# Kernel optimization log

Hardware: AMD Instinct MI355X
Metric: run time of the kernel (lower is better)

## Reference

```python
import jax, jax.numpy as jnp
import numpy as np

B, T, V, D = 128, 512, 8000, 256
H = D // 2   # per-direction LSTM hidden
L = 4        # label_dim


def setup_inputs() -> dict:
    key = jax.random.key(0)
    ks = jax.random.split(key, 16)
    s = 0.1
    pad_seq = jax.random.randint(ks[0], (B, T), 0, V)
    lens = jax.random.randint(ks[1], (B,), 1, T + 1)
    lens = lens.at[0].set(T)  # padded length == max(lens), as pad_packed_sequence would give
    emb = (jax.random.normal(ks[2], (V, D)) * s).at[0].set(0.0)  # padding_idx=0
    return {
        "pad_seq": pad_seq, "lens": lens, "emb": emb,
        "W_ih_f": jax.random.normal(ks[3], (4 * H, D)) * s,
        "W_hh_f": jax.random.normal(ks[4], (4 * H, H)) * s,
        "b_ih_f": jax.random.normal(ks[5], (4 * H,)) * s,
        "b_hh_f": jax.random.normal(ks[6], (4 * H,)) * s,
        "W_ih_b": jax.random.normal(ks[7], (4 * H, D)) * s,
        "W_hh_b": jax.random.normal(ks[8], (4 * H, H)) * s,
        "b_ih_b": jax.random.normal(ks[9], (4 * H,)) * s,
        "b_hh_b": jax.random.normal(ks[10], (4 * H,)) * s,
        "W_lab": jax.random.normal(ks[11], (L, D)) * s,
        "b_lab": jax.random.normal(ks[12], (L,)) * s,
        "transitions": jax.random.normal(ks[13], (L, L)),
        "from_BOS": jax.random.normal(ks[14], (L,)),
        "to_EOS": jax.random.normal(ks[15], (L,)),
    }


def _lstm(xs_t, mask_t, Wih, Whh, bih, bhh, reverse):
    """Masked unidirectional LSTM over time-major xs_t [T,B,D]; emulates
    pack_padded_sequence semantics (state frozen and output zeroed at pads)."""
    nb, nh = xs_t.shape[1], Whh.shape[1]

    def step(carry, inp):
        h, c = carry
        x_t, m_t = inp  # [B,D], [B,1] bool
        g = x_t @ Wih.T + bih + h @ Whh.T + bhh
        i, f, gg, o = jnp.split(g, 4, axis=-1)
        c2 = jax.nn.sigmoid(f) * c + jax.nn.sigmoid(i) * jnp.tanh(gg)
        h2 = jax.nn.sigmoid(o) * jnp.tanh(c2)
        h = jnp.where(m_t, h2, h)
        c = jnp.where(m_t, c2, c)
        return (h, c), jnp.where(m_t, h2, 0.0)

    init = (jnp.zeros((nb, nh), xs_t.dtype), jnp.zeros((nb, nh), xs_t.dtype))
    _, ys = jax.lax.scan(step, init, (xs_t, mask_t), reverse=reverse)
    return ys  # [T,B,H]


def reference(pad_seq, lens, emb, W_ih_f, W_hh_f, b_ih_f, b_hh_f,
              W_ih_b, W_hh_b, b_ih_b, b_hh_b, W_lab, b_lab,
              transitions, from_BOS, to_EOS):
    b, t = pad_seq.shape
    x = emb[pad_seq]                       # [B,T,D]
    xs_t = jnp.transpose(x, (1, 0, 2))     # [T,B,D]
    mask_t = (jnp.arange(t)[:, None] < lens[None, :])[:, :, None]  # [T,B,1]

    hf = _lstm(xs_t, mask_t, W_ih_f, W_hh_f, b_ih_f, b_hh_f, reverse=False)
    hb = _lstm(xs_t, mask_t, W_ih_b, W_hh_b, b_ih_b, b_hh_b, reverse=True)
    h = jnp.concatenate([hf, hb], axis=-1)           # [T,B,D]
    scores = h @ W_lab.T + b_lab                     # [T,B,L] emissions

    # --- Viterbi forward pass ---
    best0 = from_BOS[None, :] + scores[0]            # [B,L]

    def vstep(best, inp):
        ti, e = inp                                  # step index, emissions [B,L]
        smat = best[:, :, None] + e[:, None, :] + transitions[None]  # [B,prev,cur]
        valid = (lens > ti)[:, None]
        nb = jnp.where(valid, smat.max(axis=1), best)
        return nb, jnp.argmax(smat, axis=1)          # backtrace [B,L]

    bestT, bt = jax.lax.scan(vstep, best0, (jnp.arange(1, t), scores[1:]))
    final_vec = bestT + to_EOS[None, :]              # [B,L]
    last_lab = jnp.argmax(final_vec, axis=1)         # [B]

    # --- backtrace: label[t] = bt[t][label[t+1]] for t < len-1 ---
    bt_pad = jnp.concatenate([bt, jnp.zeros((1,) + bt.shape[1:], bt.dtype)], axis=0)  # [T,B,L]

    def bstep(cur, inp):
        ti, bt_t = inp
        cand = jnp.take_along_axis(bt_t, cur[:, None], axis=1)[:, 0]
        cur = jnp.where(ti == lens - 1, last_lab,
                        jnp.where(ti < lens - 1, cand, cur))
        return cur, cur

    _, labs = jax.lax.scan(bstep, jnp.zeros((b,), last_lab.dtype),
                           (jnp.arange(t), bt_pad), reverse=True)
    labels = labs.T  # [B,T]
    len_bool = jnp.arange(t)[None, :] < lens[:, None]
    return labels * len_bool
```

## Files before the change

kernel.cpp:

```cpp
#include <hip/hip_runtime.h>
#include <math.h>

#define VOCAB 8000
#define BATCH 128
#define TMAX  512
#define DIM   256
#define HID   128
#define G4    512
#define NCOL  1024

__device__ __forceinline__ float dpp_xor1(float x) {
  int r = __builtin_amdgcn_update_dpp(0, __builtin_bit_cast(int, x),
                                      0xB1, 0xF, 0xF, true);
  return __builtin_bit_cast(float, r);
}
__device__ __forceinline__ float dpp_xor2(float x) {
  int r = __builtin_amdgcn_update_dpp(0, __builtin_bit_cast(int, x),
                                      0x4E, 0xF, 0xF, true);
  return __builtin_bit_cast(float, r);
}
__device__ __forceinline__ unsigned dpp_xor1u(unsigned x) {
  return (unsigned)__builtin_amdgcn_update_dpp(0, (int)x, 0xB1, 0xF, 0xF, true);
}
__device__ __forceinline__ unsigned dpp_xor2u(unsigned x) {
  return (unsigned)__builtin_amdgcn_update_dpp(0, (int)x, 0x4E, 0xF, 0xF, true);
}
__device__ __forceinline__ float dpp_bc0(float x) {
  int r = __builtin_amdgcn_update_dpp(0, __builtin_bit_cast(int, x),
                                      0x00, 0xF, 0xF, true);
  return __builtin_bit_cast(float, r);
}
__device__ __forceinline__ float dpp_bc1(float x) {
  int r = __builtin_amdgcn_update_dpp(0, __builtin_bit_cast(int, x),
                                      0x55, 0xF, 0xF, true);
  return __builtin_bit_cast(float, r);
}
__device__ __forceinline__ float dpp_bc2(float x) {
  int r = __builtin_amdgcn_update_dpp(0, __builtin_bit_cast(int, x),
                                      0xAA, 0xF, 0xF, true);
  return __builtin_bit_cast(float, r);
}
__device__ __forceinline__ float dpp_bc3(float x) {
  int r = __builtin_amdgcn_update_dpp(0, __builtin_bit_cast(int, x),
                                      0xFF, 0xF, 0xF, true);
  return __builtin_bit_cast(float, r);
}

__device__ __forceinline__ void bar_lds() {
  asm volatile("s_waitcnt lgkmcnt(0)" ::: "memory");
  __builtin_amdgcn_s_barrier();
}

__global__ __launch_bounds__(256) void embw_gemm(
    const float* __restrict__ emb,
    const float* __restrict__ Wf, const float* __restrict__ Wb,
    const float* __restrict__ bihf, const float* __restrict__ bhhf,
    const float* __restrict__ bihb, const float* __restrict__ bhhb,
    float* __restrict__ embW) {
  __shared__ float As[32][132];
  __shared__ float Bs[32][132];
  const int tid = threadIdx.x;
  const int m0 = blockIdx.x * 128;
  const int n0 = blockIdx.y * 128;
  const int tx = tid & 15, ty = tid >> 4;
  const int lrow = tid >> 1;
  const int lseg = (tid & 1) * 16;
  const float* Wsrc = (n0 < 512) ? Wf : Wb;
  const int nbase = (n0 < 512) ? n0 : (n0 - 512);

  float acc[8][8];
  #pragma unroll
  for (int i = 0; i < 8; ++i)
    #pragma unroll
    for (int jj = 0; jj < 8; ++jj) acc[i][jj] = 0.f;

  for (int k0 = 0; k0 < 256; k0 += 32) {
    const int gm = m0 + lrow;
    #pragma unroll
    for (int q = 0; q < 4; ++q) {
      float4 v = make_float4(0.f, 0.f, 0.f, 0.f);
      if (gm < VOCAB) v = *(const float4*)(emb + (size_t)gm * 256 + k0 + lseg + 4 * q);
      As[lseg + 4*q + 0][lrow] = v.x;
      As[lseg + 4*q + 1][lrow] = v.y;
      As[lseg + 4*q + 2][lrow] = v.z;
      As[lseg + 4*q + 3][lrow] = v.w;
    }
    #pragma unroll
    for (int q = 0; q < 4; ++q) {
      float4 v = *(const float4*)(Wsrc + (size_t)(nbase + lrow) * 256 + k0 + lseg + 4 * q);
      Bs[lseg + 4*q + 0][lrow] = v.x;
      Bs[lseg + 4*q + 1][lrow] = v.y;
      Bs[lseg + 4*q + 2][lrow] = v.z;
      Bs[lseg + 4*q + 3][lrow] = v.w;
    }
    __syncthreads();
    #pragma unroll
    for (int k = 0; k < 32; ++k) {
      float4 av0 = *(const float4*)&As[k][ty * 8];
      float4 av1 = *(const float4*)&As[k][ty * 8 + 4];
      float4 bv0 = *(const float4*)&Bs[k][tx * 4];
      float4 bv1 = *(const float4*)&Bs[k][64 + tx * 4];
      float a[8]  = {av0.x, av0.y, av0.z, av0.w, av1.x, av1.y, av1.z, av1.w};
      float bb[8] = {bv0.x, bv0.y, bv0.z, bv0.w, bv1.x, bv1.y, bv1.z, bv1.w};
      #pragma unroll
      for (int i = 0; i < 8; ++i)
        #pragma unroll
        for (int jj = 0; jj < 8; ++jj)
          acc[i][jj] += a[i] * bb[jj];
    }
    __syncthreads();
  }

  float bias[8];
  #pragma unroll
  for (int jj = 0; jj < 8; ++jj) {
    int n = n0 + ((jj < 4) ? (tx * 4 + jj) : (64 + tx * 4 + (jj - 4)));
    bias[jj] = (n < 512) ? (bihf[n] + bhhf[n]) : (bihb[n - 512] + bhhb[n - 512]);
  }
  #pragma unroll
  for (int i = 0; i < 8; ++i) {
    int gm = m0 + ty * 8 + i;
    if (gm >= VOCAB) continue;
    float4 v0 = make_float4(acc[i][0] + bias[0], acc[i][1] + bias[1],
                            acc[i][2] + bias[2], acc[i][3] + bias[3]);
    float4 v1 = make_float4(acc[i][4] + bias[4], acc[i][5] + bias[5],
                            acc[i][6] + bias[6], acc[i][7] + bias[7]);
    *(float4*)(embW + (size_t)gm * NCOL + n0 + tx * 4) = v0;
    *(float4*)(embW + (size_t)gm * NCOL + n0 + 64 + tx * 4) = v1;
  }
}

#define REP8(M) M(0) M(1) M(2) M(3) M(4) M(5) M(6) M(7)
#define REP8G(M,G) M(G,0) M(G,1) M(G,2) M(G,3) M(G,4) M(G,5) M(G,6) M(G,7)

__global__ __launch_bounds__(512)
__attribute__((amdgpu_waves_per_eu(2, 2)))
void lstm_rec(
    const int* __restrict__ pad_seq, const int* __restrict__ lens,
    const float* __restrict__ Whh_f, const float* __restrict__ Whh_b,
    const float* __restrict__ embW, const float* __restrict__ W_lab,
    float* __restrict__ e_part) {
  const int dir = blockIdx.x & 1;
  const int b   = blockIdx.x >> 1;
  const int tid = threadIdx.x;
  const int j   = tid >> 2;
  const int q   = tid & 3;
  const int parity = q & 1;
  const int half   = (q >> 1) & 1;

  __shared__ float ring[8][4][36];
  __shared__ float wls[4][132];
  __shared__ int   tok[TMAX];

  tok[tid] = pad_seq[b * TMAX + tid];
  wls[tid >> 7][tid & 127] = W_lab[(tid >> 7) * DIM + dir * HID + (tid & 127)];
  if (tid < 144) ((float*)ring)[tid] = 0.f;

  const int len = lens[b];
  const float* __restrict__ Whh = dir ? Whh_b : Whh_f;

  const float4* wr0 = (const float4*)(Whh + (size_t)(0 * HID + j) * HID + 32 * q);
  const float4* wr1 = (const float4*)(Whh + (size_t)(1 * HID + j) * HID + 32 * q);
  const float4* wr2 = (const float4*)(Whh + (size_t)(2 * HID + j) * HID + 32 * q);
  const float4* wr3 = (const float4*)(Whh + (size_t)(3 * HID + j) * HID + 32 * q);
#define DECLW(G,I)                                                      \
  float w##G##_##I##_0, w##G##_##I##_1, w##G##_##I##_2, w##G##_##I##_3; \
  { float4 t = wr##G[I];                                                \
    w##G##_##I##_0 = t.x; w##G##_##I##_1 = t.y;                         \
    w##G##_##I##_2 = t.z; w##G##_##I##_3 = t.w; }                       \
  asm volatile("" : "+v"(w##G##_##I##_0));                              \
  asm volatile("" : "+v"(w##G##_##I##_1));                              \
  asm volatile("" : "+v"(w##G##_##I##_2));                              \
  asm volatile("" : "+v"(w##G##_##I##_3));
  REP8G(DECLW,0) REP8G(DECLW,1) REP8G(DECLW,2) REP8G(DECLW,3)
#undef DECLW

#define KEEPW(G,I)                                                      \
  asm volatile("" : "+v"(w##G##_##I##_0), "+v"(w##G##_##I##_1),         \
                    "+v"(w##G##_##I##_2), "+v"(w##G##_##I##_3));

  float c = 0.f;
  const float ascale = (q == 2) ? 2.f : 1.f;
  const float* __restrict__ ecol = embW + dir * G4 + (q * HID + j);
  float* __restrict__ ep = e_part + (size_t)(dir * BATCH + b) * TMAX * 4;

  bar_lds();

  float xb0, xb1, xb2, xb3, xb4, xb5, xb6, xb7;
#define PRE(r) { const int ss = nbase + r; xb##r = 0.f;                 \
    if (ss < len) {                                                     \
      const int tt = dir ? (len - 1 - ss) : ss;                         \
      xb##r = ecol[(size_t)tok[tt] * NCOL]; } }
  { const int nbase = 0; REP8(PRE) }

#define MACC(G,I)                                         \
    a##G##0 = fmaf(hv##I.x, w##G##_##I##_0, a##G##0);     \
    a##G##1 = fmaf(hv##I.y, w##G##_##I##_1, a##G##1);     \
    a##G##2 = fmaf(hv##I.z, w##G##_##I##_2, a##G##2);     \
    a##G##3 = fmaf(hv##I.w, w##G##_##I##_3, a##G##3);

#define STEP(r, XW)                                                     \
  {                                                                     \
    const float4* h4 = (const float4*)&ring[r][q][0];                   \
    float4 hv0 = h4[0], hv1 = h4[1], hv2 = h4[2], hv3 = h4[3];          \
    float4 hv4 = h4[4], hv5 = h4[5], hv6 = h4[6], hv7 = h4[7];          \
    float a00=0.f,a01=0.f,a02=0.f,a03=0.f;                              \
    float a10=0.f,a11=0.f,a12=0.f,a13=0.f;                              \
    float a20=0.f,a21=0.f,a22=0.f,a23=0.f;                              \
    float a30=0.f,a31=0.f,a32=0.f,a33=0.f;                              \
    REP8G(MACC,0) REP8G(MACC,1) REP8G(MACC,2) REP8G(MACC,3)             \
    const float p0 = (a00+a01)+(a02+a03);                               \
    const float p1 = (a10+a11)+(a12+a13);                               \
    const float p2 = (a20+a21)+(a22+a23);                               \
    const float p3 = (a30+a31)+(a32+a33);                               \
     \
    const float klo = parity ? p1 : p0, slo = parity ? p0 : p1;         \
    const float khi = parity ? p3 : p2, shi = parity ? p2 : p3;         \
    const float alo = klo + dpp_xor1(slo);                              \
    const float ahi = khi + dpp_xor1(shi);                              \
    const float kb = half ? ahi : alo, sb = half ? alo : ahi;           \
    const float tot = kb + dpp_xor2(sb);                                \
    const float aa = tot + (XW);                                        \
    const float sg = 1.f / (1.f + __expf(-ascale * aa));                \
    const float act = (q == 2) ? (2.f * sg - 1.f) : sg;                 \
                          \
    const float e1 = dpp_xor1(act);                                     \
    const float e2 = dpp_xor2(act);                                     \
    const float e3 = dpp_xor2(e1);                                      \
    const float ev  = parity ? e1 : act, od  = parity ? act : e1;       \
    const float ev2 = parity ? e3 : e2,  od2 = parity ? e2 : e3;        \
    const float ig = half ? ev2 : ev, fg = half ? od2 : od;             \
    const float gt = half ? ev : ev2, og = half ? od : od2;             \
    c = fg * c + ig * gt;                                               \
    const float s2 = 1.f / (1.f + __expf(-2.f * c));                    \
    const float hh = og * (2.f * s2 - 1.f);                             \
    if (q == 0) ring[(r + 1) & 7][j >> 5][j & 31] = hh;                 \
    bar_lds();                                                          \
  }

  for (int s0 = 0; s0 < len; s0 += 8) {
    REP8G(KEEPW,0) REP8G(KEEPW,1) REP8G(KEEPW,2) REP8G(KEEPW,3)
    const int cnt = (len - s0 < 8) ? (len - s0) : 8;
    STEP(0, xb0)
    if (cnt > 1) STEP(1, xb1)
    if (cnt > 2) STEP(2, xb2)
    if (cnt > 3) STEP(3, xb3)
    if (cnt > 4) STEP(4, xb4)
    if (cnt > 5) STEP(5, xb5)
    if (cnt > 6) STEP(6, xb6)
    if (cnt > 7) STEP(7, xb7)
    { const int nbase = s0 + 8; REP8(PRE) }
    {
      const int r = tid >> 6, l = (tid >> 4) & 3, sub = tid & 15;
      if (r < cnt) {
        const float4* hp = (const float4*)&ring[(r + 1) & 7][sub >> 2][8 * (sub & 3)];
        const float4 h0 = hp[0], h1 = hp[1];
        const float4* wp = (const float4*)&wls[l][8 * sub];
        const float4 u0 = wp[0], u1 = wp[1];
        float d = h0.x*u0.x + h0.y*u0.y + h0.z*u0.z + h0.w*u0.w
                + h1.x*u1.x + h1.y*u1.y + h1.z*u1.z + h1.w*u1.w;
        d += dpp_xor1(d); d += dpp_xor2(d);
        d += __shfl_xor(d, 4); d += __shfl_xor(d, 8);
        if (sub == 0) {
          const int ss = s0 + r;
          const int tt = dir ? (len - 1 - ss) : ss;
          ep[tt * 4 + l] = d;
        }
      }
    }
    bar_lds();
  }
#undef STEP
#undef MACC
#undef PRE
#undef KEEPW
}

__global__ __launch_bounds__(512) void viterbi_k(
    const int* __restrict__ lens, const float* __restrict__ e_part,
    const float* __restrict__ b_lab, const float* __restrict__ trans,
    const float* __restrict__ from_BOS, const float* __restrict__ to_EOS,
    int* __restrict__ out) {
  const int b = blockIdx.x;
  const int tid = threadIdx.x;
  __shared__ float sc[TMAX][4];
  __shared__ unsigned btm[TMAX];
  __shared__ int labs[TMAX];
  const int len = lens[b];

  if (tid < len) {
    const float4 f  = *(const float4*)(e_part + ((size_t)b * TMAX + tid) * 4);
    const float4 g2 = *(const float4*)(e_part + ((size_t)(BATCH + b) * TMAX + tid) * 4);
    const float4 bl = *(const float4*)b_lab;
    sc[tid][0] = f.x + g2.x + bl.x;
    sc[tid][1] = f.y + g2.y + bl.y;
    sc[tid][2] = f.z + g2.z + bl.z;
    sc[tid][3] = f.w + g2.w + bl.w;
  }
  __syncthreads();

  if (tid < 4) {
    const int l = tid;
    float trc0 = trans[0 * 4 + l], trc1 = trans[1 * 4 + l];
    float trc2 = trans[2 * 4 + l], trc3 = trans[3 * 4 + l];
    float best = from_BOS[l] + sc[0][l];
    float e_next = sc[1][l];
    for (int ti = 1; ti < len; ++ti) {
      const float e = e_next;
      e_next = sc[(ti + 1 < TMAX) ? ti + 1 : ti][l];
      const float b0 = dpp_bc0(best);
      const float b1 = dpp_bc1(best);
      const float b2 = dpp_bc2(best);
      const float b3 = dpp_bc3(best);
      float m = (b0 + e) + trc0; int arg = 0;
      float v;
      v = (b1 + e) + trc1; if (v > m) { m = v; arg = 1; }
      v = (b2 + e) + trc2; if (v > m) { m = v; arg = 2; }
      v = (b3 + e) + trc3; if (v > m) { m = v; arg = 3; }
      best = m;
      unsigned av = ((unsigned)arg) << (8 * l);
      av |= dpp_xor1u(av);
      av |= dpp_xor2u(av);
      if (l == 0) btm[ti] = av;
    }
    const float f0 = dpp_bc0(best) + to_EOS[0];
    const float f1 = dpp_bc1(best) + to_EOS[1];
    const float f2 = dpp_bc2(best) + to_EOS[2];
    const float f3 = dpp_bc3(best) + to_EOS[3];
    if (l == 0) {
      float m = f0; int last = 0;
      if (f1 > m) { m = f1; last = 1; }
      if (f2 > m) { m = f2; last = 2; }
      if (f3 > m) { m = f3; last = 3; }
      labs[len - 1] = last;
      int cur = last;
      #pragma unroll 4
      for (int ti = len - 2; ti >= 0; --ti) {
        cur = (int)((btm[ti + 1] >> (8 * cur)) & 255u);
        labs[ti] = cur;
      }
    }
  }
  __syncthreads();
  out[b * TMAX + tid] = (tid < len) ? labs[tid] : 0;
}

extern "C" void kernel_launch(void* const* d_in, const int* in_sizes, int n_in,
                              void* d_out, int out_size, void* d_ws, size_t ws_size,
                              hipStream_t stream) {
  const int*   pad_seq  = (const int*)d_in[0];
  const int*   lens     = (const int*)d_in[1];
  const float* emb      = (const float*)d_in[2];
  const float* W_ih_f   = (const float*)d_in[3];
  const float* W_hh_f   = (const float*)d_in[4];
  const float* b_ih_f   = (const float*)d_in[5];
  const float* b_hh_f   = (const float*)d_in[6];
  const float* W_ih_b   = (const float*)d_in[7];
  const float* W_hh_b   = (const float*)d_in[8];
  const float* b_ih_b   = (const float*)d_in[9];
  const float* b_hh_b   = (const float*)d_in[10];
  const float* W_lab    = (const float*)d_in[11];
  const float* b_lab    = (const float*)d_in[12];
  const float* trans    = (const float*)d_in[13];
  const float* from_BOS = (const float*)d_in[14];
  const float* to_EOS   = (const float*)d_in[15];
  int* out = (int*)d_out;

  float* embW   = (float*)d_ws;
  float* e_part = embW + (size_t)VOCAB * NCOL;

  embw_gemm<<<dim3(63, 8), 256, 0, stream>>>(emb, W_ih_f, W_ih_b,
                                             b_ih_f, b_hh_f, b_ih_b, b_hh_b, embW);
  lstm_rec<<<dim3(2 * BATCH), 512, 0, stream>>>(pad_seq, lens, W_hh_f, W_hh_b,
                                                embW, W_lab, e_part);
  viterbi_k<<<dim3(BATCH), 512, 0, stream>>>(lens, e_part, b_lab, trans,
                                             from_BOS, to_EOS, out);
}
```

Before: 577.3 us.

## Repartition LSTM recurrent matvec to two hidden units per 8-lane group

Each 8-lane group now computes two hidden units, with every lane holding a 16-wide K slice for all four gates of both units. Previously each 4-lane group handled one unit over a 32-wide slice. The h vector in LDS is re-laid out with padding per 16-wide slice, so each lane reads 4 float4s instead of 8. The cross-lane reduction gains a third stage, done with a ds_swizzle xor-4, and the output-projection shuffles also switch to ds_swizzle. The aim is to halve per-step LDS reads of h, at the cost of a longer reduction chain and serial FMA dependence chains per accumulator.

```diff
diff --git a/kernel.cpp b/kernel.cpp
--- a/kernel.cpp
+++ b/kernel.cpp
@@ -43,6 +43,14 @@
 __device__ __forceinline__ float dpp_bc3(float x) {
   int r = __builtin_amdgcn_update_dpp(0, __builtin_bit_cast(int, x),
                                       0xFF, 0xF, 0xF, true);
+  return __builtin_bit_cast(float, r);
+}
+__device__ __forceinline__ float swz_xor4(float x) {
+  int r = __builtin_amdgcn_ds_swizzle(__builtin_bit_cast(int, x), 0x101F);
+  return __builtin_bit_cast(float, r);
+}
+__device__ __forceinline__ float swz_xor8(float x) {
+  int r = __builtin_amdgcn_ds_swizzle(__builtin_bit_cast(int, x), 0x201F);
   return __builtin_bit_cast(float, r);
 }
 
@@ -131,7 +139,9 @@
 }
 
 #define REP8(M) M(0) M(1) M(2) M(3) M(4) M(5) M(6) M(7)
-#define REP8G(M,G) M(G,0) M(G,1) M(G,2) M(G,3) M(G,4) M(G,5) M(G,6) M(G,7)
+#define REPI(M,G,U) M(G,U,0) M(G,U,1) M(G,U,2) M(G,U,3)
+#define REPROW(M) REPI(M,0,0) REPI(M,1,0) REPI(M,2,0) REPI(M,3,0) \
+                  REPI(M,0,1) REPI(M,1,1) REPI(M,2,1) REPI(M,3,1)
 
 __global__ __launch_bounds__(512)
 __attribute__((amdgpu_waves_per_eu(2, 2)))
@@ -143,46 +153,53 @@
   const int dir = blockIdx.x & 1;
   const int b   = blockIdx.x >> 1;
   const int tid = threadIdx.x;
-  const int j   = tid >> 2;
-  const int q   = tid & 3;
-  const int parity = q & 1;
-  const int half   = (q >> 1) & 1;
-
-  __shared__ float ring[8][4][36];
+  const int oct = tid & 7;
+  const int grp2 = 2 * (tid >> 3);
+  const int o0 = oct & 1, o1b = (oct >> 1) & 1, o2b = (oct >> 2) & 1;
+  const int q = oct & 3;
+  const int parity = o0;
+  const int half   = o1b;
+
+  __shared__ float ring[8][160];
   __shared__ float wls[4][132];
   __shared__ int   tok[TMAX];
 
   tok[tid] = pad_seq[b * TMAX + tid];
   wls[tid >> 7][tid & 127] = W_lab[(tid >> 7) * DIM + dir * HID + (tid & 127)];
-  if (tid < 144) ((float*)ring)[tid] = 0.f;
+  if (tid < 160) ((float*)ring)[tid] = 0.f;
 
   const int len = lens[b];
   const float* __restrict__ Whh = dir ? Whh_b : Whh_f;
 
-  const float4* wr0 = (const float4*)(Whh + (size_t)(0 * HID + j) * HID + 32 * q);
-  const float4* wr1 = (const float4*)(Whh + (size_t)(1 * HID + j) * HID + 32 * q);
-  const float4* wr2 = (const float4*)(Whh + (size_t)(2 * HID + j) * HID + 32 * q);
-  const float4* wr3 = (const float4*)(Whh + (size_t)(3 * HID + j) * HID + 32 * q);
-#define DECLW(G,I)                                                      \
-  float w##G##_##I##_0, w##G##_##I##_1, w##G##_##I##_2, w##G##_##I##_3; \
-  { float4 t = wr##G[I];                                                \
-    w##G##_##I##_0 = t.x; w##G##_##I##_1 = t.y;                         \
-    w##G##_##I##_2 = t.z; w##G##_##I##_3 = t.w; }                       \
-  asm volatile("" : "+v"(w##G##_##I##_0));                              \
-  asm volatile("" : "+v"(w##G##_##I##_1));                              \
-  asm volatile("" : "+v"(w##G##_##I##_2));                              \
-  asm volatile("" : "+v"(w##G##_##I##_3));
-  REP8G(DECLW,0) REP8G(DECLW,1) REP8G(DECLW,2) REP8G(DECLW,3)
+#define DECLROW(G,U)                                                    \
+  const float4* wr##G##U = (const float4*)(Whh +                        \
+      (size_t)((G) * HID + grp2 + (U)) * HID + 16 * oct);
+  DECLROW(0,0) DECLROW(1,0) DECLROW(2,0) DECLROW(3,0)
+  DECLROW(0,1) DECLROW(1,1) DECLROW(2,1) DECLROW(3,1)
+#undef DECLROW
+#define DECLW(G,U,I)                                                    \
+  float w##G##U##_##I##_0, w##G##U##_##I##_1,                           \
+        w##G##U##_##I##_2, w##G##U##_##I##_3;                           \
+  { float4 t = wr##G##U[I];                                             \
+    w##G##U##_##I##_0 = t.x; w##G##U##_##I##_1 = t.y;                   \
+    w##G##U##_##I##_2 = t.z; w##G##U##_##I##_3 = t.w; }                 \
+  asm volatile("" : "+v"(w##G##U##_##I##_0));                           \
+  asm volatile("" : "+v"(w##G##U##_##I##_1));                           \
+  asm volatile("" : "+v"(w##G##U##_##I##_2));                           \
+  asm volatile("" : "+v"(w##G##U##_##I##_3));
+  REPROW(DECLW)
 #undef DECLW
 
-#define KEEPW(G,I)                                                      \
-  asm volatile("" : "+v"(w##G##_##I##_0), "+v"(w##G##_##I##_1),         \
-                    "+v"(w##G##_##I##_2), "+v"(w##G##_##I##_3));
+#define KEEPW(G,U,I)                                                    \
+  asm volatile("" : "+v"(w##G##U##_##I##_0), "+v"(w##G##U##_##I##_1),   \
+                    "+v"(w##G##U##_##I##_2), "+v"(w##G##U##_##I##_3));
 
   float c = 0.f;
   const float ascale = (q == 2) ? 2.f : 1.f;
-  const float* __restrict__ ecol = embW + dir * G4 + (q * HID + j);
+  const float* __restrict__ ecol = embW + dir * G4 + q * HID + grp2 + o2b;
   float* __restrict__ ep = e_part + (size_t)(dir * BATCH + b) * TMAX * 4;
+  const int nunit = grp2 + o2b;
+  const int hoff  = 20 * (nunit >> 4) + (nunit & 15);
 
   bar_lds();
 
@@ -193,33 +210,35 @@
       xb##r = ecol[(size_t)tok[tt] * NCOL]; } }
   { const int nbase = 0; REP8(PRE) }
 
-#define MACC(G,I)                                         \
-    a##G##0 = fmaf(hv##I.x, w##G##_##I##_0, a##G##0);     \
-    a##G##1 = fmaf(hv##I.y, w##G##_##I##_1, a##G##1);     \
-    a##G##2 = fmaf(hv##I.z, w##G##_##I##_2, a##G##2);     \
-    a##G##3 = fmaf(hv##I.w, w##G##_##I##_3, a##G##3);
+#define MACC(G,U,I)                                                     \
+    a##G##U = fmaf(hv##I.x, w##G##U##_##I##_0, a##G##U);                \
+    a##G##U = fmaf(hv##I.y, w##G##U##_##I##_1, a##G##U);                \
+    a##G##U = fmaf(hv##I.z, w##G##U##_##I##_2, a##G##U);                \
+    a##G##U = fmaf(hv##I.w, w##G##U##_##I##_3, a##G##U);
 
 #define STEP(r, XW)                                                     \
   {                                                                     \
-    const float4* h4 = (const float4*)&ring[r][q][0];                   \
+    const float4* h4 = (const float4*)&ring[r][20 * oct];               \
     float4 hv0 = h4[0], hv1 = h4[1], hv2 = h4[2], hv3 = h4[3];          \
-    float4 hv4 = h4[4], hv5 = h4[5], hv6 = h4[6], hv7 = h4[7];          \
-    float a00=0.f,a01=0.f,a02=0.f,a03=0.f;                              \
-    float a10=0.f,a11=0.f,a12=0.f,a13=0.f;                              \
-    float a20=0.f,a21=0.f,a22=0.f,a23=0.f;                              \
-    float a30=0.f,a31=0.f,a32=0.f,a33=0.f;                              \
-    REP8G(MACC,0) REP8G(MACC,1) REP8G(MACC,2) REP8G(MACC,3)             \
-    const float p0 = (a00+a01)+(a02+a03);                               \
-    const float p1 = (a10+a11)+(a12+a13);                               \
-    const float p2 = (a20+a21)+(a22+a23);                               \
-    const float p3 = (a30+a31)+(a32+a33);                               \
-     \
-    const float klo = parity ? p1 : p0, slo = parity ? p0 : p1;         \
-    const float khi = parity ? p3 : p2, shi = parity ? p2 : p3;         \
-    const float alo = klo + dpp_xor1(slo);                              \
-    const float ahi = khi + dpp_xor1(shi);                              \
-    const float kb = half ? ahi : alo, sb = half ? alo : ahi;           \
-    const float tot = kb + dpp_xor2(sb);                                \
+    float a00=0.f,a10=0.f,a20=0.f,a30=0.f;                              \
+    float a01=0.f,a11=0.f,a21=0.f,a31=0.f;                              \
+    REPROW(MACC)                                                        \
+                  \
+    float t0, t1;                                                       \
+    t0 = o0 ? a10 : a00; t1 = o0 ? a00 : a10;                           \
+    const float b0 = t0 + dpp_xor1(t1);                                 \
+    t0 = o0 ? a30 : a20; t1 = o0 ? a20 : a30;                           \
+    const float b1 = t0 + dpp_xor1(t1);                                 \
+    t0 = o0 ? a11 : a01; t1 = o0 ? a01 : a11;                           \
+    const float b2 = t0 + dpp_xor1(t1);                                 \
+    t0 = o0 ? a31 : a21; t1 = o0 ? a21 : a31;                           \
+    const float b3 = t0 + dpp_xor1(t1);                                 \
+    t0 = o1b ? b1 : b0; t1 = o1b ? b0 : b1;                             \
+    const float c0s = t0 + dpp_xor2(t1);                                \
+    t0 = o1b ? b3 : b2; t1 = o1b ? b2 : b3;                             \
+    const float c1s = t0 + dpp_xor2(t1);                                \
+    t0 = o2b ? c1s : c0s; t1 = o2b ? c0s : c1s;                         \
+    const float tot = t0 + swz_xor4(t1);                                \
     const float aa = tot + (XW);                                        \
     const float sg = 1.f / (1.f + __expf(-ascale * aa));                \
     const float act = (q == 2) ? (2.f * sg - 1.f) : sg;                 \
@@ -234,12 +253,12 @@
     c = fg * c + ig * gt;                                               \
     const float s2 = 1.f / (1.f + __expf(-2.f * c));                    \
     const float hh = og * (2.f * s2 - 1.f);                             \
-    if (q == 0) ring[(r + 1) & 7][j >> 5][j & 31] = hh;                 \
+    if (q == 0) ring[(r + 1) & 7][hoff] = hh;                           \
     bar_lds();                                                          \
   }
 
   for (int s0 = 0; s0 < len; s0 += 8) {
-    REP8G(KEEPW,0) REP8G(KEEPW,1) REP8G(KEEPW,2) REP8G(KEEPW,3)
+    REPROW(KEEPW)
     const int cnt = (len - s0 < 8) ? (len - s0) : 8;
     STEP(0, xb0)
     if (cnt > 1) STEP(1, xb1)
@@ -253,14 +272,15 @@
     {
       const int r = tid >> 6, l = (tid >> 4) & 3, sub = tid & 15;
       if (r < cnt) {
-        const float4* hp = (const float4*)&ring[(r + 1) & 7][sub >> 2][8 * (sub & 3)];
+        const float4* hp = (const float4*)
+            &ring[(r + 1) & 7][20 * (sub >> 1) + 8 * (sub & 1)];
         const float4 h0 = hp[0], h1 = hp[1];
         const float4* wp = (const float4*)&wls[l][8 * sub];
         const float4 u0 = wp[0], u1 = wp[1];
         float d = h0.x*u0.x + h0.y*u0.y + h0.z*u0.z + h0.w*u0.w
                 + h1.x*u1.x + h1.y*u1.y + h1.z*u1.z + h1.w*u1.w;
         d += dpp_xor1(d); d += dpp_xor2(d);
-        d += __shfl_xor(d, 4); d += __shfl_xor(d, 8);
+        d += swz_xor4(d); d += swz_xor8(d);
         if (sub == 0) {
           const int ss = s0 + r;
           const int tt = dir ? (len - 1 - ss) : ss;
```

Measured after the change: 578.1 us. No clear change (+0.1%).

## Split each LSTM gate's hidden-state dot product across two threads

Applied to the files above, without the earlier changes.

The recurrent kernel now runs 1024 threads per block instead of 512. Eight threads serve each hidden unit: each handles one gate and half of the 128-long recurrent dot product, so it holds 64 recurrent weights in registers instead of 128. This halves the serial FMA chain per thread on the per-step critical path. A single DPP add combines the two halves, and the gate exchange now uses xor-2 and xor-4 lane swizzles, adding a new helper. In exchange, every per-step barrier must synchronise twice as many waves, and more threads repeat the nonlinearities.

```diff
diff --git a/kernel.cpp b/kernel.cpp
--- a/kernel.cpp
+++ b/kernel.cpp
@@ -17,6 +17,12 @@
 __device__ __forceinline__ float dpp_xor2(float x) {
   int r = __builtin_amdgcn_update_dpp(0, __builtin_bit_cast(int, x),
                                       0x4E, 0xF, 0xF, true);
+  return __builtin_bit_cast(float, r);
+}
+__device__ __forceinline__ float dpp_xor4(float x) {
+  int t = __builtin_amdgcn_update_dpp(0, __builtin_bit_cast(int, x),
+                                      0x1B, 0xF, 0xF, true);
+  int r = __builtin_amdgcn_update_dpp(0, t, 0x141, 0xF, 0xF, true);
   return __builtin_bit_cast(float, r);
 }
 __device__ __forceinline__ unsigned dpp_xor1u(unsigned x) {
@@ -131,10 +137,10 @@
 }
 
 #define REP8(M) M(0) M(1) M(2) M(3) M(4) M(5) M(6) M(7)
-#define REP8G(M,G) M(G,0) M(G,1) M(G,2) M(G,3) M(G,4) M(G,5) M(G,6) M(G,7)
-
-__global__ __launch_bounds__(512)
-__attribute__((amdgpu_waves_per_eu(2, 2)))
+#define REP16(M) M(0) M(1) M(2) M(3) M(4) M(5) M(6) M(7) \
+                 M(8) M(9) M(10) M(11) M(12) M(13) M(14) M(15)
+
+__global__ __launch_bounds__(1024, 4)
 void lstm_rec(
     const int* __restrict__ pad_seq, const int* __restrict__ lens,
     const float* __restrict__ Whh_f, const float* __restrict__ Whh_b,
@@ -143,45 +149,44 @@
   const int dir = blockIdx.x & 1;
   const int b   = blockIdx.x >> 1;
   const int tid = threadIdx.x;
-  const int j   = tid >> 2;
-  const int q   = tid & 3;
-  const int parity = q & 1;
-  const int half   = (q >> 1) & 1;
+  const int j   = tid >> 3;
+  const int s   = tid & 7;
+  const int g   = s >> 1;
+  const int kh  = s & 1;
+  const int parity = g & 1;
+  const int half   = g >> 1;
 
   __shared__ float ring[8][4][36];
   __shared__ float wls[4][132];
   __shared__ int   tok[TMAX];
 
-  tok[tid] = pad_seq[b * TMAX + tid];
-  wls[tid >> 7][tid & 127] = W_lab[(tid >> 7) * DIM + dir * HID + (tid & 127)];
+  if (tid < TMAX) tok[tid] = pad_seq[b * TMAX + tid];
+  if (tid < 512)
+    wls[tid >> 7][tid & 127] = W_lab[(tid >> 7) * DIM + dir * HID + (tid & 127)];
   if (tid < 144) ((float*)ring)[tid] = 0.f;
 
   const int len = lens[b];
   const float* __restrict__ Whh = dir ? Whh_b : Whh_f;
 
-  const float4* wr0 = (const float4*)(Whh + (size_t)(0 * HID + j) * HID + 32 * q);
-  const float4* wr1 = (const float4*)(Whh + (size_t)(1 * HID + j) * HID + 32 * q);
-  const float4* wr2 = (const float4*)(Whh + (size_t)(2 * HID + j) * HID + 32 * q);
-  const float4* wr3 = (const float4*)(Whh + (size_t)(3 * HID + j) * HID + 32 * q);
-#define DECLW(G,I)                                                      \
-  float w##G##_##I##_0, w##G##_##I##_1, w##G##_##I##_2, w##G##_##I##_3; \
-  { float4 t = wr##G[I];                                                \
-    w##G##_##I##_0 = t.x; w##G##_##I##_1 = t.y;                         \
-    w##G##_##I##_2 = t.z; w##G##_##I##_3 = t.w; }                       \
-  asm volatile("" : "+v"(w##G##_##I##_0));                              \
-  asm volatile("" : "+v"(w##G##_##I##_1));                              \
-  asm volatile("" : "+v"(w##G##_##I##_2));                              \
-  asm volatile("" : "+v"(w##G##_##I##_3));
-  REP8G(DECLW,0) REP8G(DECLW,1) REP8G(DECLW,2) REP8G(DECLW,3)
+  const float4* wr = (const float4*)(Whh + (size_t)(g * HID + j) * HID + kh * 64);
+#define DECLW(I)                                                        \
+  float w##I##_0, w##I##_1, w##I##_2, w##I##_3;                         \
+  { float4 t = wr[I];                                                   \
+    w##I##_0 = t.x; w##I##_1 = t.y; w##I##_2 = t.z; w##I##_3 = t.w; }   \
+  asm volatile("" : "+v"(w##I##_0));                                    \
+  asm volatile("" : "+v"(w##I##_1));                                    \
+  asm volatile("" : "+v"(w##I##_2));                                    \
+  asm volatile("" : "+v"(w##I##_3));
+  REP16(DECLW)
 #undef DECLW
 
-#define KEEPW(G,I)                                                      \
-  asm volatile("" : "+v"(w##G##_##I##_0), "+v"(w##G##_##I##_1),         \
-                    "+v"(w##G##_##I##_2), "+v"(w##G##_##I##_3));
+#define KEEPW(I)                                                        \
+  asm volatile("" : "+v"(w##I##_0), "+v"(w##I##_1),                     \
+                    "+v"(w##I##_2), "+v"(w##I##_3));
 
   float c = 0.f;
-  const float ascale = (q == 2) ? 2.f : 1.f;
-  const float* __restrict__ ecol = embW + dir * G4 + (q * HID + j);
+  const float ascale = (g == 2) ? 2.f : 1.f;
+  const float* __restrict__ ecol = embW + dir * G4 + (g * HID + j);
   float* __restrict__ ep = e_part + (size_t)(dir * BATCH + b) * TMAX * 4;
 
   bar_lds();
@@ -193,40 +198,34 @@
       xb##r = ecol[(size_t)tok[tt] * NCOL]; } }
   { const int nbase = 0; REP8(PRE) }
 
-#define MACC(G,I)                                         \
-    a##G##0 = fmaf(hv##I.x, w##G##_##I##_0, a##G##0);     \
-    a##G##1 = fmaf(hv##I.y, w##G##_##I##_1, a##G##1);     \
-    a##G##2 = fmaf(hv##I.z, w##G##_##I##_2, a##G##2);     \
-    a##G##3 = fmaf(hv##I.w, w##G##_##I##_3, a##G##3);
+#define MACCA(I)                                                        \
+  { float4 hv = hA[I];                                                  \
+    a0 = fmaf(hv.x, w##I##_0, a0); a1 = fmaf(hv.y, w##I##_1, a1);       \
+    a2 = fmaf(hv.z, w##I##_2, a2); a3 = fmaf(hv.w, w##I##_3, a3); }
+#define MACCB(I, I8)                                                    \
+  { float4 hv = hB[I];                                                  \
+    a0 = fmaf(hv.x, w##I8##_0, a0); a1 = fmaf(hv.y, w##I8##_1, a1);     \
+    a2 = fmaf(hv.z, w##I8##_2, a2); a3 = fmaf(hv.w, w##I8##_3, a3); }
 
 #define STEP(r, XW)                                                     \
   {                                                                     \
-    const float4* h4 = (const float4*)&ring[r][q][0];                   \
-    float4 hv0 = h4[0], hv1 = h4[1], hv2 = h4[2], hv3 = h4[3];          \
-    float4 hv4 = h4[4], hv5 = h4[5], hv6 = h4[6], hv7 = h4[7];          \
-    float a00=0.f,a01=0.f,a02=0.f,a03=0.f;                              \
-    float a10=0.f,a11=0.f,a12=0.f,a13=0.f;                              \
-    float a20=0.f,a21=0.f,a22=0.f,a23=0.f;                              \
-    float a30=0.f,a31=0.f,a32=0.f,a33=0.f;                              \
-    REP8G(MACC,0) REP8G(MACC,1) REP8G(MACC,2) REP8G(MACC,3)             \
-    const float p0 = (a00+a01)+(a02+a03);                               \
-    const float p1 = (a10+a11)+(a12+a13);                               \
-    const float p2 = (a20+a21)+(a22+a23);                               \
-    const float p3 = (a30+a31)+(a32+a33);                               \
-     \
-    const float klo = parity ? p1 : p0, slo = parity ? p0 : p1;         \
-    const float khi = parity ? p3 : p2, shi = parity ? p2 : p3;         \
-    const float alo = klo + dpp_xor1(slo);                              \
-    const float ahi = khi + dpp_xor1(shi);                              \
-    const float kb = half ? ahi : alo, sb = half ? alo : ahi;           \
-    const float tot = kb + dpp_xor2(sb);                                \
+    const float4* hA = (const float4*)&ring[r][2 * kh][0];              \
+    const float4* hB = (const float4*)&ring[r][2 * kh + 1][0];          \
+    float a0 = 0.f, a1 = 0.f, a2 = 0.f, a3 = 0.f;                       \
+    MACCA(0) MACCA(1) MACCA(2) MACCA(3)                                 \
+    MACCA(4) MACCA(5) MACCA(6) MACCA(7)                                 \
+    MACCB(0, 8)  MACCB(1, 9)  MACCB(2, 10) MACCB(3, 11)                 \
+    MACCB(4, 12) MACCB(5, 13) MACCB(6, 14) MACCB(7, 15)                 \
+    const float p = (a0 + a1) + (a2 + a3);                              \
+               \
+    const float tot = p + dpp_xor1(p);                                  \
     const float aa = tot + (XW);                                        \
     const float sg = 1.f / (1.f + __expf(-ascale * aa));                \
-    const float act = (q == 2) ? (2.f * sg - 1.f) : sg;                 \
-                          \
-    const float e1 = dpp_xor1(act);                                     \
-    const float e2 = dpp_xor2(act);                                     \
-    const float e3 = dpp_xor2(e1);                                      \
+    const float act = (g == 2) ? (2.f * sg - 1.f) : sg;                 \
+     \
+    const float e1 = dpp_xor2(act);                                     \
+    const float e2 = dpp_xor4(act);                                     \
+    const float e3 = dpp_xor4(e1);                                      \
     const float ev  = parity ? e1 : act, od  = parity ? act : e1;       \
     const float ev2 = parity ? e3 : e2,  od2 = parity ? e2 : e3;        \
     const float ig = half ? ev2 : ev, fg = half ? od2 : od;             \
@@ -234,12 +233,12 @@
     c = fg * c + ig * gt;                                               \
     const float s2 = 1.f / (1.f + __expf(-2.f * c));                    \
     const float hh = og * (2.f * s2 - 1.f);                             \
-    if (q == 0) ring[(r + 1) & 7][j >> 5][j & 31] = hh;                 \
+    if (s == 0) ring[(r + 1) & 7][j >> 5][j & 31] = hh;                 \
     bar_lds();                                                          \
   }
 
   for (int s0 = 0; s0 < len; s0 += 8) {
-    REP8G(KEEPW,0) REP8G(KEEPW,1) REP8G(KEEPW,2) REP8G(KEEPW,3)
+    REP16(KEEPW)
     const int cnt = (len - s0 < 8) ? (len - s0) : 8;
     STEP(0, xb0)
     if (cnt > 1) STEP(1, xb1)
@@ -271,7 +270,8 @@
     bar_lds();
   }
 #undef STEP
-#undef MACC
+#undef MACCA
+#undef MACCB
 #undef PRE
 #undef KEEPW
 }
@@ -371,8 +371,8 @@
 
   embw_gemm<<<dim3(63, 8), 256, 0, stream>>>(emb, W_ih_f, W_ih_b,
                                              b_ih_f, b_hh_f, b_ih_b, b_hh_b, embW);
-  lstm_rec<<<dim3(2 * BATCH), 512, 0, stream>>>(pad_seq, lens, W_hh_f, W_hh_b,
-                                                embW, W_lab, e_part);
+  lstm_rec<<<dim3(2 * BATCH), 1024, 0, stream>>>(pad_seq, lens, W_hh_f, W_hh_b,
+                                                 embW, W_lab, e_part);
   viterbi_k<<<dim3(BATCH), 512, 0, stream>>>(lens, e_part, b_lab, trans,
                                              from_BOS, to_EOS, out);
 }
```

Measured after the change: 722.2 us. +25.1%, slower.

## Process two batch rows per LSTM block to share register-resident weights

Applied to the files above, without the earlier changes.

Each recurrent block now handles two sequences (b and b+64) for one direction, interleaving their steps so both use the same W_hh held in registers and share one barrier per step. The grid shrinks from 256 to 128 blocks. The aim is to hide per-step latency through independent work and halve the number of weight loads, at the cost of fewer blocks on a large GPU and more serialized arithmetic per step. The serial length per block becomes the longer of the two sequences.

```diff
diff --git a/kernel.cpp b/kernel.cpp
--- a/kernel.cpp
+++ b/kernel.cpp
@@ -141,22 +141,32 @@
     const float* __restrict__ embW, const float* __restrict__ W_lab,
     float* __restrict__ e_part) {
   const int dir = blockIdx.x & 1;
-  const int b   = blockIdx.x >> 1;
+  const int bp  = blockIdx.x >> 1;
+  const int b0  = bp;
+  const int b1  = bp + 64;
   const int tid = threadIdx.x;
   const int j   = tid >> 2;
   const int q   = tid & 3;
   const int parity = q & 1;
   const int half   = (q >> 1) & 1;
 
-  __shared__ float ring[8][4][36];
+  __shared__ float ringA[8][4][36];
+  __shared__ float ringB[8][4][36];
   __shared__ float wls[4][132];
-  __shared__ int   tok[TMAX];
-
-  tok[tid] = pad_seq[b * TMAX + tid];
+  __shared__ int   tokA[TMAX];
+  __shared__ int   tokB[TMAX];
+
+  tokA[tid] = pad_seq[b0 * TMAX + tid];
+  tokB[tid] = pad_seq[b1 * TMAX + tid];
   wls[tid >> 7][tid & 127] = W_lab[(tid >> 7) * DIM + dir * HID + (tid & 127)];
-  if (tid < 144) ((float*)ring)[tid] = 0.f;
-
-  const int len = lens[b];
+  if (tid < 144) {
+    ((float*)ringA)[tid] = 0.f;
+    ((float*)ringB)[tid] = 0.f;
+  }
+
+  const int lenA = lens[b0];
+  const int lenB = lens[b1];
+  const int lenM = (lenA > lenB) ? lenA : lenB;
   const float* __restrict__ Whh = dir ? Whh_b : Whh_f;
 
   const float4* wr0 = (const float4*)(Whh + (size_t)(0 * HID + j) * HID + 32 * q);
@@ -179,19 +189,25 @@
   asm volatile("" : "+v"(w##G##_##I##_0), "+v"(w##G##_##I##_1),         \
                     "+v"(w##G##_##I##_2), "+v"(w##G##_##I##_3));
 
-  float c = 0.f;
+  float cAv = 0.f, cBv = 0.f;
   const float ascale = (q == 2) ? 2.f : 1.f;
   const float* __restrict__ ecol = embW + dir * G4 + (q * HID + j);
-  float* __restrict__ ep = e_part + (size_t)(dir * BATCH + b) * TMAX * 4;
+  float* __restrict__ epA = e_part + (size_t)(dir * BATCH + b0) * TMAX * 4;
+  float* __restrict__ epB = e_part + (size_t)(dir * BATCH + b1) * TMAX * 4;
 
   bar_lds();
 
+  float xa0, xa1, xa2, xa3, xa4, xa5, xa6, xa7;
   float xb0, xb1, xb2, xb3, xb4, xb5, xb6, xb7;
-#define PRE(r) { const int ss = nbase + r; xb##r = 0.f;                 \
-    if (ss < len) {                                                     \
-      const int tt = dir ? (len - 1 - ss) : ss;                         \
-      xb##r = ecol[(size_t)tok[tt] * NCOL]; } }
-  { const int nbase = 0; REP8(PRE) }
+#define PREA(r) { const int ss = nbase + r; xa##r = 0.f;                \
+    if (ss < lenA) {                                                    \
+      const int tt = dir ? (lenA - 1 - ss) : ss;                        \
+      xa##r = ecol[(size_t)tokA[tt] * NCOL]; } }
+#define PREB(r) { const int ss = nbase + r; xb##r = 0.f;                \
+    if (ss < lenB) {                                                    \
+      const int tt = dir ? (lenB - 1 - ss) : ss;                        \
+      xb##r = ecol[(size_t)tokB[tt] * NCOL]; } }
+  { const int nbase = 0; REP8(PREA) REP8(PREB) }
 
 #define MACC(G,I)                                         \
     a##G##0 = fmaf(hv##I.x, w##G##_##I##_0, a##G##0);     \
@@ -199,9 +215,9 @@
     a##G##2 = fmaf(hv##I.z, w##G##_##I##_2, a##G##2);     \
     a##G##3 = fmaf(hv##I.w, w##G##_##I##_3, a##G##3);
 
-#define STEP(r, XW)                                                     \
+#define STEP1(r, XW, RING, CV, HWSTMT)                                  \
   {                                                                     \
-    const float4* h4 = (const float4*)&ring[r][q][0];                   \
+    const float4* h4 = (const float4*)&RING[r][q][0];                   \
     float4 hv0 = h4[0], hv1 = h4[1], hv2 = h4[2], hv3 = h4[3];          \
     float4 hv4 = h4[4], hv5 = h4[5], hv6 = h4[6], hv7 = h4[7];          \
     float a00=0.f,a01=0.f,a02=0.f,a03=0.f;                              \
@@ -213,7 +229,6 @@
     const float p1 = (a10+a11)+(a12+a13);                               \
     const float p2 = (a20+a21)+(a22+a23);                               \
     const float p3 = (a30+a31)+(a32+a33);                               \
-     \
     const float klo = parity ? p1 : p0, slo = parity ? p0 : p1;         \
     const float khi = parity ? p3 : p2, shi = parity ? p2 : p3;         \
     const float alo = klo + dpp_xor1(slo);                              \
@@ -223,7 +238,6 @@
     const float aa = tot + (XW);                                        \
     const float sg = 1.f / (1.f + __expf(-ascale * aa));                \
     const float act = (q == 2) ? (2.f * sg - 1.f) : sg;                 \
-                          \
     const float e1 = dpp_xor1(act);                                     \
     const float e2 = dpp_xor2(act);                                     \
     const float e3 = dpp_xor2(e1);                                      \
@@ -231,48 +245,74 @@
     const float ev2 = parity ? e3 : e2,  od2 = parity ? e2 : e3;        \
     const float ig = half ? ev2 : ev, fg = half ? od2 : od;             \
     const float gt = half ? ev : ev2, og = half ? od : od2;             \
-    c = fg * c + ig * gt;                                               \
-    const float s2 = 1.f / (1.f + __expf(-2.f * c));                    \
+    CV = fg * CV + ig * gt;                                             \
+    const float s2 = 1.f / (1.f + __expf(-2.f * CV));                   \
     const float hh = og * (2.f * s2 - 1.f);                             \
-    if (q == 0) ring[(r + 1) & 7][j >> 5][j & 31] = hh;                 \
-    bar_lds();                                                          \
-  }
-
-  for (int s0 = 0; s0 < len; s0 += 8) {
+    HWSTMT                                                              \
+  }
+
+#define HWA(r) if (q == 0) ringA[((r) + 1) & 7][j >> 5][j & 31] = hh;
+#define HWB(r) if (q == 0) ringB[((r) + 1) & 7][j >> 5][j & 31] = hh;
+
+#define DO(r)                                                           \
+  {                                                                     \
+    const bool dA = (cntA > r), dB = (cntB > r);     \
+    if (dA && dB) { STEP1(r, xa##r, ringA, cAv, HWA(r))                 \
+                    STEP1(r, xb##r, ringB, cBv, HWB(r)) }               \
+    else if (dA)  { STEP1(r, xa##r, ringA, cAv, HWA(r)) }               \
+    else if (dB)  { STEP1(r, xb##r, ringB, cBv, HWB(r)) }               \
+    if (dA || dB) bar_lds();                                            \
+  }
+
+  for (int s0 = 0; s0 < lenM; s0 += 8) {
     REP8G(KEEPW,0) REP8G(KEEPW,1) REP8G(KEEPW,2) REP8G(KEEPW,3)
-    const int cnt = (len - s0 < 8) ? (len - s0) : 8;
-    STEP(0, xb0)
-    if (cnt > 1) STEP(1, xb1)
-    if (cnt > 2) STEP(2, xb2)
-    if (cnt > 3) STEP(3, xb3)
-    if (cnt > 4) STEP(4, xb4)
-    if (cnt > 5) STEP(5, xb5)
-    if (cnt > 6) STEP(6, xb6)
-    if (cnt > 7) STEP(7, xb7)
-    { const int nbase = s0 + 8; REP8(PRE) }
+    const int remA = lenA - s0, remB = lenB - s0;
+    const int cntA = (remA < 0) ? 0 : ((remA < 8) ? remA : 8);
+    const int cntB = (remB < 0) ? 0 : ((remB < 8) ? remB : 8);
+    DO(0) DO(1) DO(2) DO(3) DO(4) DO(5) DO(6) DO(7)
+    { const int nbase = s0 + 8; REP8(PREA) REP8(PREB) }
     {
       const int r = tid >> 6, l = (tid >> 4) & 3, sub = tid & 15;
-      if (r < cnt) {
-        const float4* hp = (const float4*)&ring[(r + 1) & 7][sub >> 2][8 * (sub & 3)];
+      if (r < cntA) {
+        const float4* hp = (const float4*)&ringA[(r + 1) & 7][sub >> 2][8 * (sub & 3)];
         const float4 h0 = hp[0], h1 = hp[1];
         const float4* wp = (const float4*)&wls[l][8 * sub];
         const float4 u0 = wp[0], u1 = wp[1];
         float d = h0.x*u0.x + h0.y*u0.y + h0.z*u0.z + h0.w*u0.w
                 + h1.x*u1.x + h1.y*u1.y + h1.z*u1.z + h1.w*u1.w;
-        d += dpp_xor1(d); d += dpp_xor2(d);
+        d += __shfl_xor(d, 1); d += __shfl_xor(d, 2);
         d += __shfl_xor(d, 4); d += __shfl_xor(d, 8);
         if (sub == 0) {
           const int ss = s0 + r;
-          const int tt = dir ? (len - 1 - ss) : ss;
-          ep[tt * 4 + l] = d;
+          const int tt = dir ? (lenA - 1 - ss) : ss;
+          epA[tt * 4 + l] = d;
         }
       }
+      if (r < cntB) {
+        const float4* hp = (const float4*)&ringB[(r + 1) & 7][sub >> 2][8 * (sub & 3)];
+        const float4 h0 = hp[0], h1 = hp[1];
+        const float4* wp = (const float4*)&wls[l][8 * sub];
+        const float4 u0 = wp[0], u1 = wp[1];
+        float d = h0.x*u0.x + h0.y*u0.y + h0.z*u0.z + h0.w*u0.w
+                + h1.x*u1.x + h1.y*u1.y + h1.z*u1.z + h1.w*u1.w;
+        d += __shfl_xor(d, 1); d += __shfl_xor(d, 2);
+        d += __shfl_xor(d, 4); d += __shfl_xor(d, 8);
+        if (sub == 0) {
+          const int ss = s0 + r;
+          const int tt = dir ? (lenB - 1 - ss) : ss;
+          epB[tt * 4 + l] = d;
+        }
+      }
     }
     bar_lds();
   }
-#undef STEP
+#undef DO
+#undef HWA
+#undef HWB
+#undef STEP1
 #undef MACC
-#undef PRE
+#undef PREA
+#undef PREB
 #undef KEEPW
 }
 
@@ -371,8 +411,8 @@
 
   embw_gemm<<<dim3(63, 8), 256, 0, stream>>>(emb, W_ih_f, W_ih_b,
                                              b_ih_f, b_hh_f, b_ih_b, b_hh_b, embW);
-  lstm_rec<<<dim3(2 * BATCH), 512, 0, stream>>>(pad_seq, lens, W_hh_f, W_hh_b,
-                                                embW, W_lab, e_part);
+  lstm_rec<<<dim3(128), 512, 0, stream>>>(pad_seq, lens, W_hh_f, W_hh_b,
+                                          embW, W_lab, e_part);
   viterbi_k<<<dim3(BATCH), 512, 0, stream>>>(lens, e_part, b_lab, trans,
                                              from_BOS, to_EOS, out);
 }
```

Measured after the change: 818.6 us. +41.8%, slower.
